# Kernel optimization log

Hardware: AMD Instinct MI355X
Metric: run time of the kernel (lower is better)

Reference implementation:

```python
import jax, jax.numpy as jnp
import numpy as np

BB, F, K, D, H, HFF, L, M_PREV = 128, 8, 256, 256, 256, 512, 2, 2


def setup_inputs() -> dict:
    key = jax.random.key(0)
    ks = jax.random.split(key, 16)
    f32 = jnp.float32

    def lin(k, fan_in, shape):
        return (jax.random.normal(k, shape, dtype=f32) / np.sqrt(fan_in)).astype(f32)

    inp = {
        "x_BD": jax.random.normal(ks[0], (BB, D), dtype=f32),
        "xhat_BFD": jax.random.normal(ks[1], (BB, F, D), dtype=f32),
        "codes_MBF": jax.random.randint(ks[2], (M_PREV, BB, 1), 0, F * K, dtype=jnp.int64),
        "codebook": jax.random.normal(ks[3], (K, D), dtype=f32) / np.sqrt(D),
        "W_in": lin(ks[4], D, (D, H)),
        "b_in": jnp.zeros((H,), f32),
        # concat projection over cat([h, xhat], -1): (H + D) -> H
        "W_cat": lin(ks[5], H + D, (H + D, H)),
        "b_cat": jnp.zeros((H,), f32),
        "W1": lin(ks[6], H, (L, H, HFF)),
        "b1": jnp.zeros((L, HFF), f32),
        "W2": lin(ks[7], HFF, (L, HFF, H)),
        "b2": jnp.zeros((L, H), f32),
        "W_out": lin(ks[8], H, (H, D)),
        "b_out": jnp.zeros((D,), f32),
    }
    return inp


def reference(x_BD, xhat_BFD, codes_MBF, codebook, W_in, b_in, W_cat, b_cat,
              W1, b1, W2, b2, W_out, b_out):
    Bb, Fb, Dd = xhat_BFD.shape
    Kk = codebook.shape[0]

    # in_proj applied to the (shared) codebook once: [K, H]
    h0 = codebook @ W_in + b_in

    # concat(h, xhat) as a linear over the concatenation, split to avoid
    # materializing a [Bb,F,K,H+D] tensor.
    Wc, Wx = W_cat[:H], W_cat[H:]
    h = (h0 @ Wc)[None, None] + (xhat_BFD @ Wx)[:, :, None] + b_cat  # [Bb,F,K,H]

    # residual MLP blocks: h <- h + W2 relu(W1 h)
    for l in range(L):
        h = h + jax.nn.relu(h @ W1[l] + b1[l]) @ W2[l] + b2[l]

    # out_proj + residual codeword (res_codeword_coeff = 1.0) + xhat offset
    cw = h @ W_out + b_out + codebook[None, None]        # [Bb,F,K,D]
    cw = cw + xhat_BFD[:, :, None]                        # reconstructed candidates

    cflat = cw.reshape(Bb, Fb * Kk, Dd)                   # [Bb, F*K, D]

    dists = (jnp.sum(x_BD * x_BD, -1, keepdims=True)
             - 2.0 * jnp.einsum('bd,bkd->bk', x_BD, cflat)
             + jnp.sum(cflat * cflat, -1))                # [Bb, F*K]

    idx = jnp.argmin(dists, axis=-1)                      # [Bb]
    xhat_next_BFD = jnp.take_along_axis(cflat, idx[:, None, None], axis=1)  # [Bb,1,D]

    codes_new = jnp.concatenate(
        [codes_MBF, idx[None, :, None].astype(codes_MBF.dtype)], axis=0)
    return xhat_next_BFD, codes_new
```

## Files before the change

kernel.cpp:

```cpp
#include <hip/hip_runtime.h>
#include <hip/hip_bf16.h>

#define B_   128
#define F_   8
#define K_   256
#define D_   256
#define H_   256
#define HFF_ 512
#define RT   64

typedef _Float16 half8  __attribute__((ext_vector_type(8)));
typedef _Float16 half4v __attribute__((ext_vector_type(4)));
typedef float floatx4   __attribute__((ext_vector_type(4)));

#define MFMAH(a,b,c) __builtin_amdgcn_mfma_f32_16x16x32_f16(a,b,c,0,0,0)

#define HA_S  260
#define HMA_S 132

__global__ void k_prep(const float* __restrict__ cb, const float* __restrict__ Win,
                       const float* __restrict__ bin, const float* __restrict__ Wcat,
                       const float* __restrict__ bcat, const float* __restrict__ xhat,
                       const float* __restrict__ W1, const float* __restrict__ W2,
                       const float* __restrict__ Wout,
                       float* __restrict__ u, float* __restrict__ v,
                       _Float16* __restrict__ w1f, _Float16* __restrict__ w2f,
                       _Float16* __restrict__ wof) {
  const int blk = blockIdx.x, t = threadIdx.x;
  if (blk < K_) {
    __shared__ float row[D_];
    __shared__ float h0row[H_];
    row[t] = cb[blk * D_ + t];
    __syncthreads();
    float acc = bin[t];
    #pragma unroll 4
    for (int i = 0; i < D_; ++i) acc = fmaf(row[i], Win[i * H_ + t], acc);
    h0row[t] = acc;
    __syncthreads();
    float acc2 = 0.f;
    #pragma unroll 4
    for (int i = 0; i < H_; ++i) acc2 = fmaf(h0row[i], Wcat[i * H_ + t], acc2);
    u[blk * H_ + t] = acc2;
  } else if (blk < K_ + B_ * F_) {
    __shared__ float row2[D_];
    const int bf = blk - K_;
    row2[t] = xhat[bf * D_ + t];
    __syncthreads();
    float acc = bcat[t];
    #pragma unroll 4
    for (int i = 0; i < D_; ++i) acc = fmaf(row2[i], Wcat[(H_ + i) * H_ + t], acc);
    v[bf * H_ + t] = acc;
  } else {
    const int e = (blk - (K_ + B_ * F_)) * 256 + t;
    const float* src; _Float16* dst; int N, NT, le;
    if (e < 262144) {
      const int layer = e >> 17; le = e & 131071;
      src = W1 + layer * (H_ * HFF_); dst = w1f + layer * (H_ * HFF_);
      N = HFF_; NT = 32;
    } else if (e < 524288) {
      const int e2 = e - 262144;
      const int layer = e2 >> 17; le = e2 & 131071;
      src = W2 + layer * (HFF_ * H_); dst = w2f + layer * (HFF_ * H_);
      N = H_; NT = 16;
    } else {
      le = e - 524288; src = Wout; dst = wof; N = D_; NT = 16;
    }
    const int jj = le & 7, lane = (le >> 3) & 63, r = le >> 9;
    const int ntile = r % NT, kstep = r / NT;
    const int row = kstep * 32 + (lane >> 4) * 8 + jj;
    const int colc = ntile * 16 + (lane & 15);
    dst[le] = (_Float16)src[row * N + colc];
  }
}

__global__ __launch_bounds__(256, 3) void k_main(
    const float* __restrict__ u, const float* __restrict__ v,
    const _Float16* __restrict__ w1f, const float* __restrict__ b1,
    const _Float16* __restrict__ w2f, const float* __restrict__ b2,
    const _Float16* __restrict__ woutf, const float* __restrict__ bout,
    const float* __restrict__ cb, const float* __restrict__ xhat,
    const float* __restrict__ x, float* __restrict__ dists) {
  __shared__ _Float16 hA[64][HA_S];
  __shared__ _Float16 hmA[64][HMA_S];
  __shared__ float x_s[D_], xh_s[D_];
  __shared__ float dist_s[4][64];

  const int t = threadIdx.x;
  const int blk = blockIdx.x;
  const int bf = blk >> 2, k0 = (blk & 3) << 6;
  const int b = bf >> 3, f = bf & 7;
  const int wave = t >> 6, lane = t & 63;
  const int col = lane & 15, quad = lane >> 4;
  const int lane8 = lane * 8;

  x_s[t]  = x[b * D_ + t];
  xh_s[t] = xhat[bf * D_ + t];

  {
    const int r = t >> 2, c0 = (t & 3) * 64;
    const float* up = u + (k0 + r) * H_ + c0;
    const float* vp = v + bf * H_ + c0;
    #pragma unroll
    for (int j = 0; j < 64; j += 8) {
      float4 uA = *(const float4*)(up + j);
      float4 vA = *(const float4*)(vp + j);
      float4 uB = *(const float4*)(up + j + 4);
      float4 vB = *(const float4*)(vp + j + 4);
      half8 hv8;
      hv8[0] = (_Float16)(uA.x + vA.x); hv8[1] = (_Float16)(uA.y + vA.y);
      hv8[2] = (_Float16)(uA.z + vA.z); hv8[3] = (_Float16)(uA.w + vA.w);
      hv8[4] = (_Float16)(uB.x + vB.x); hv8[5] = (_Float16)(uB.y + vB.y);
      hv8[6] = (_Float16)(uB.z + vB.z); hv8[7] = (_Float16)(uB.w + vB.w);
      *(half8*)&hA[r][c0 + j] = hv8;
    }
  }
  __syncthreads();

  const floatx4 zero4 = {0.f, 0.f, 0.f, 0.f};

  #pragma unroll 1
  for (int l = 0; l < 2; ++l) {
    const _Float16* w1_l = w1f + l * (H_ * HFF_);
    const _Float16* w2_l = w2f + l * (HFF_ * H_);
    const float* b1l = b1 + l * HFF_;
    const float* b2l = b2 + l * H_;

    floatx4 acc2[4][4];
    #pragma unroll
    for (int mt = 0; mt < 4; ++mt)
      #pragma unroll
      for (int nt = 0; nt < 4; ++nt) acc2[mt][nt] = zero4;

    #pragma unroll 1
    for (int ch = 0; ch < 4; ++ch) {
      floatx4 acc1[2][4];
      #pragma unroll
      for (int mt = 0; mt < 2; ++mt)
        #pragma unroll
        for (int nt = 0; nt < 4; ++nt) acc1[mt][nt] = zero4;

      const _Float16* w1_b = w1_l + (ch * 8 + wave * 2) * 512 + lane8;

      #pragma unroll 4
      for (int ks = 0; ks < 8; ++ks) {
        half8 b0 = *(const half8*)&hA[col][ks * 32 + quad * 8];
        half8 b1v = *(const half8*)&hA[16 + col][ks * 32 + quad * 8];
        half8 b2v = *(const half8*)&hA[32 + col][ks * 32 + quad * 8];
        half8 b3v = *(const half8*)&hA[48 + col][ks * 32 + quad * 8];
        const int ko = ks * 32 * 512;
        #pragma unroll
        for (int mt = 0; mt < 2; ++mt) {
          half8 aw = *(const half8*)(w1_b + ko + mt * 512);
          acc1[mt][0] = MFMAH(aw, b0, acc1[mt][0]);
          acc1[mt][1] = MFMAH(aw, b1v, acc1[mt][1]);
          acc1[mt][2] = MFMAH(aw, b2v, acc1[mt][2]);
          acc1[mt][3] = MFMAH(aw, b3v, acc1[mt][3]);
        }
      }
      #pragma unroll
      for (int mt = 0; mt < 2; ++mt) {
        const int floc = (wave * 2 + mt) * 16 + quad * 4;
        float4 bb = *(const float4*)&b1l[ch * 128 + floc];
        #pragma unroll
        for (int nt = 0; nt < 4; ++nt) {
          const int row = nt * 16 + col;
          half4v nh;
          #pragma unroll
          for (int p = 0; p < 4; ++p)
            nh[p] = (_Float16)fmaxf(acc1[mt][nt][p] + ((const float*)&bb)[p], 0.f);
          *(half4v*)&hmA[row][floc] = nh;
        }
      }
      __syncthreads();

      const _Float16* w2_b = w2_l + (ch * 64 + wave * 4) * 512 + lane8;
      #pragma unroll 2
      for (int ks = 0; ks < 4; ++ks) {
        half8 b0 = *(const half8*)&hmA[col][ks * 32 + quad * 8];
        half8 b1v = *(const half8*)&hmA[16 + col][ks * 32 + quad * 8];
        half8 b2v = *(const half8*)&hmA[32 + col][ks * 32 + quad * 8];
        half8 b3v = *(const half8*)&hmA[48 + col][ks * 32 + quad * 8];
        const int ko = ks * 16 * 512;
        #pragma unroll
        for (int mt = 0; mt < 4; ++mt) {
          half8 aw = *(const half8*)(w2_b + ko + mt * 512);
          acc2[mt][0] = MFMAH(aw, b0, acc2[mt][0]);
          acc2[mt][1] = MFMAH(aw, b1v, acc2[mt][1]);
          acc2[mt][2] = MFMAH(aw, b2v, acc2[mt][2]);
          acc2[mt][3] = MFMAH(aw, b3v, acc2[mt][3]);
        }
      }
      __syncthreads();
    }

    #pragma unroll
    for (int mt = 0; mt < 4; ++mt) {
      const int feat0 = (wave * 4 + mt) * 16 + quad * 4;
      float4 bb = *(const float4*)&b2l[feat0];
      #pragma unroll
      for (int nt = 0; nt < 4; ++nt) {
        const int row = nt * 16 + col;
        half4v oh = *(half4v*)&hA[row][feat0];
        half4v nh;
        #pragma unroll
        for (int p = 0; p < 4; ++p)
          nh[p] = (_Float16)((float)oh[p] + acc2[mt][nt][p] + ((const float*)&bb)[p]);
        *(half4v*)&hA[row][feat0] = nh;
      }
    }
    __syncthreads();
  }

  floatx4 acc3[4][4];
  #pragma unroll
  for (int mt = 0; mt < 4; ++mt)
    #pragma unroll
    for (int nt = 0; nt < 4; ++nt) acc3[mt][nt] = zero4;

  const _Float16* wo_b = woutf + (wave * 4) * 512 + lane8;
  #pragma unroll 2
  for (int ks = 0; ks < 8; ++ks) {
    half8 b0 = *(const half8*)&hA[col][ks * 32 + quad * 8];
    half8 b1v = *(const half8*)&hA[16 + col][ks * 32 + quad * 8];
    half8 b2v = *(const half8*)&hA[32 + col][ks * 32 + quad * 8];
    half8 b3v = *(const half8*)&hA[48 + col][ks * 32 + quad * 8];
    const int ko = ks * 16 * 512;
    #pragma unroll
    for (int mt = 0; mt < 4; ++mt) {
      half8 aw = *(const half8*)(wo_b + ko + mt * 512);
      acc3[mt][0] = MFMAH(aw, b0, acc3[mt][0]);
      acc3[mt][1] = MFMAH(aw, b1v, acc3[mt][1]);
      acc3[mt][2] = MFMAH(aw, b2v, acc3[mt][2]);
      acc3[mt][3] = MFMAH(aw, b3v, acc3[mt][3]);
    }
  }

  float s[4] = {0.f, 0.f, 0.f, 0.f};
  #pragma unroll
  for (int mt = 0; mt < 4; ++mt) {
    const int d0 = (wave * 4 + mt) * 16 + quad * 4;
    float4 bo = *(const float4*)&bout[d0];
    float4 xv = *(const float4*)&x_s[d0];
    float4 xh4 = *(const float4*)&xh_s[d0];
    #pragma unroll
    for (int nt = 0; nt < 4; ++nt) {
      float4 cbv = *(const float4*)&cb[(k0 + nt * 16 + col) * D_ + d0];
      #pragma unroll
      for (int p = 0; p < 4; ++p) {
        float base = ((const float*)&bo)[p] + ((const float*)&xh4)[p];
        float xx = ((const float*)&xv)[p];
        float cw = acc3[mt][nt][p] + base + ((const float*)&cbv)[p];
        s[nt] += cw * (cw - 2.f * xx);
      }
    }
  }
  #pragma unroll
  for (int nt = 0; nt < 4; ++nt) {
    s[nt] += __shfl_xor(s[nt], 16, 64);
    s[nt] += __shfl_xor(s[nt], 32, 64);
  }
  if (quad == 0) {
    #pragma unroll
    for (int nt = 0; nt < 4; ++nt)
      dist_s[wave][nt * 16 + col] = s[nt];
  }
  __syncthreads();
  if (t < 64) {
    float d = dist_s[0][t] + dist_s[1][t] + dist_s[2][t] + dist_s[3][t];
    dists[b * (F_ * K_) + f * K_ + k0 + t] = d;
  }
}

__global__ void k_top8(const float* __restrict__ dists, int* __restrict__ topi) {
  __shared__ float ds[F_ * K_];
  __shared__ float bv[256];
  __shared__ int bi_s[256];
  const int b = blockIdx.x, t = threadIdx.x;
  for (int j = t; j < F_ * K_; j += 256) ds[j] = dists[b * (F_ * K_) + j];
  __syncthreads();
  for (int pass = 0; pass < 8; ++pass) {
    float best = 3.4e38f; int bi = 0;
    for (int j = t; j < F_ * K_; j += 256) {
      const float dv = ds[j];
      if (dv < best) { best = dv; bi = j; }
    }
    bv[t] = best; bi_s[t] = bi;
    __syncthreads();
    for (int s = 128; s > 0; s >>= 1) {
      if (t < s) {
        const float ov = bv[t + s]; const int oi = bi_s[t + s];
        if (ov < bv[t] || (ov == bv[t] && oi < bi_s[t])) { bv[t] = ov; bi_s[t] = oi; }
      }
      __syncthreads();
    }
    if (t == 0) { topi[b * 8 + pass] = bi_s[0]; ds[bi_s[0]] = 3.4e38f; }
    __syncthreads();
  }
}

__global__ void k_rescore(const float* __restrict__ u, const float* __restrict__ v,
                          const float* __restrict__ W1, const float* __restrict__ b1,
                          const float* __restrict__ W2, const float* __restrict__ b2,
                          const float* __restrict__ Wout, const float* __restrict__ bout,
                          const float* __restrict__ cb, const float* __restrict__ xhat,
                          const float* __restrict__ x, const int* __restrict__ topi,
                          float* __restrict__ resc) {
  __shared__ float hs[H_];
  __shared__ float hms[HFF_];
  __shared__ float red[256];
  const int bc = blockIdx.x, t = threadIdx.x;
  const int b = bc >> 3;
  const int idx = topi[bc];
  const int f = idx >> 8, k = idx & 255;
  const int bf = b * F_ + f;

  hs[t] = u[k * H_ + t] + v[bf * H_ + t];
  __syncthreads();
  for (int l = 0; l < 2; ++l) {
    const float* W1l = W1 + l * (H_ * HFF_);
    const float* W2l = W2 + l * (HFF_ * H_);
    float a0 = b1[l * HFF_ + t], a1 = b1[l * HFF_ + 256 + t];
    for (int i = 0; i < H_; ++i) {
      const float hv = hs[i];
      a0 = fmaf(hv, W1l[i * HFF_ + t], a0);
      a1 = fmaf(hv, W1l[i * HFF_ + 256 + t], a1);
    }
    hms[t] = fmaxf(a0, 0.f);
    hms[t + 256] = fmaxf(a1, 0.f);
    __syncthreads();
    float hn = hs[t] + b2[l * H_ + t];
    for (int jj = 0; jj < HFF_; ++jj)
      hn = fmaf(hms[jj], W2l[jj * H_ + t], hn);
    __syncthreads();
    hs[t] = hn;
    __syncthreads();
  }
  float cw = bout[t] + cb[k * D_ + t] + xhat[bf * D_ + t];
  for (int i = 0; i < H_; ++i) cw = fmaf(hs[i], Wout[i * D_ + t], cw);
  red[t] = cw * (cw - 2.f * x[b * D_ + t]);
  __syncthreads();
  for (int s = 128; s > 0; s >>= 1) {
    if (t < s) red[t] += red[t + s];
    __syncthreads();
  }
  if (t == 0) resc[bc] = red[0];
}

__global__ void k_final(const float* __restrict__ u, const float* __restrict__ v,
                        const float* __restrict__ W1, const float* __restrict__ b1,
                        const float* __restrict__ W2, const float* __restrict__ b2,
                        const float* __restrict__ Wout, const float* __restrict__ bout,
                        const float* __restrict__ cb, const float* __restrict__ xhat,
                        const int* __restrict__ codes, const int* __restrict__ topi,
                        const float* __restrict__ resc, float* __restrict__ out) {
  __shared__ float hs[H_];
  __shared__ float hms[HFF_];
  __shared__ int idx_sh;
  const int b = blockIdx.x, t = threadIdx.x;
  if (t == 0) {
    float bd = 3.4e38f; int bidx = 1 << 30;
    for (int c = 0; c < 8; ++c) {
      const float d = resc[b * 8 + c];
      const int ix = topi[b * 8 + c];
      if (d < bd || (d == bd && ix < bidx)) { bd = d; bidx = ix; }
    }
    idx_sh = bidx;
  }
  __syncthreads();
  const int idx = idx_sh;
  const int f = idx >> 8, k = idx & 255;
  const int bf = b * F_ + f;

  hs[t] = u[k * H_ + t] + v[bf * H_ + t];
  __syncthreads();
  for (int l = 0; l < 2; ++l) {
    const float* W1l = W1 + l * (H_ * HFF_);
    const float* W2l = W2 + l * (HFF_ * H_);
    float a0 = b1[l * HFF_ + t], a1 = b1[l * HFF_ + 256 + t];
    for (int i = 0; i < H_; ++i) {
      const float hv = hs[i];
      a0 = fmaf(hv, W1l[i * HFF_ + t], a0);
      a1 = fmaf(hv, W1l[i * HFF_ + 256 + t], a1);
    }
    hms[t] = fmaxf(a0, 0.f);
    hms[t + 256] = fmaxf(a1, 0.f);
    __syncthreads();
    float hn = hs[t] + b2[l * H_ + t];
    for (int jj = 0; jj < HFF_; ++jj)
      hn = fmaf(hms[jj], W2l[jj * H_ + t], hn);
    __syncthreads();
    hs[t] = hn;
    __syncthreads();
  }
  float cw = bout[t] + cb[k * D_ + t] + xhat[bf * D_ + t];
  for (int i = 0; i < H_; ++i) cw = fmaf(hs[i], Wout[i * D_ + t], cw);

  out[b * D_ + t] = cw;
  if (t < 2)
    out[B_ * D_ + t * B_ + b] = (float)codes[t * B_ + b];
  else if (t == 2)
    out[B_ * D_ + 2 * B_ + b] = (float)idx;
}

extern "C" void kernel_launch(void* const* d_in, const int* in_sizes, int n_in,
                              void* d_out, int out_size, void* d_ws, size_t ws_size,
                              hipStream_t stream) {
  const float* x    = (const float*)d_in[0];
  const float* xhat = (const float*)d_in[1];
  const int*   codes= (const int*)d_in[2];
  const float* cb   = (const float*)d_in[3];
  const float* Win  = (const float*)d_in[4];
  const float* bin  = (const float*)d_in[5];
  const float* Wcat = (const float*)d_in[6];
  const float* bcat = (const float*)d_in[7];
  const float* W1   = (const float*)d_in[8];
  const float* b1   = (const float*)d_in[9];
  const float* W2   = (const float*)d_in[10];
  const float* b2   = (const float*)d_in[11];
  const float* Wout = (const float*)d_in[12];
  const float* bout = (const float*)d_in[13];
  float* out = (float*)d_out;

  float* u     = (float*)d_ws;
  float* v     = u + K_ * H_;
  float* dists = v + B_ * F_ * H_;
  float* resc  = dists + B_ * F_ * K_;
  int*   topi  = (int*)(resc + 1024);
  int*   pad   = topi + 1024;
  _Float16* w1f  = (_Float16*)(pad + 128);
  _Float16* w2f  = w1f + 2 * H_ * HFF_;
  _Float16* wof  = w2f + 2 * HFF_ * H_;

  k_prep<<<K_ + B_ * F_ + 2304, 256, 0, stream>>>(cb, Win, bin, Wcat, bcat, xhat,
                                                  W1, W2, Wout, u, v, w1f, w2f, wof);

  k_main<<<B_ * F_ * (K_ / RT), 256, 0, stream>>>(u, v, w1f, b1, w2f, b2,
                                                  wof, bout, cb, xhat, x, dists);
  k_top8<<<B_, 256, 0, stream>>>(dists, topi);
  k_rescore<<<B_ * 8, 256, 0, stream>>>(u, v, W1, b1, W2, b2, Wout, bout, cb, xhat,
                                        x, topi, resc);
  k_final<<<B_, 256, 0, stream>>>(u, v, W1, b1, W2, b2, Wout, bout, cb, xhat,
                                  codes, topi, resc, out);
}
```

Measured before the change: 562.3 us.

## Double-buffer FFN hidden chunks and widen main kernel to eight waves

```diff
diff --git a/kernel.cpp b/kernel.cpp
--- a/kernel.cpp
+++ b/kernel.cpp
@@ -73,7 +73,7 @@
   }
 }
 
-__global__ __launch_bounds__(256, 3) void k_main(
+__global__ __launch_bounds__(512, 4) void k_main(
     const float* __restrict__ u, const float* __restrict__ v,
     const _Float16* __restrict__ w1f, const float* __restrict__ b1,
     const _Float16* __restrict__ w2f, const float* __restrict__ b2,
@@ -81,9 +81,9 @@
     const float* __restrict__ cb, const float* __restrict__ xhat,
     const float* __restrict__ x, float* __restrict__ dists) {
   __shared__ _Float16 hA[64][HA_S];
-  __shared__ _Float16 hmA[64][HMA_S];
+  __shared__ _Float16 hmA[2][64][HMA_S];
   __shared__ float x_s[D_], xh_s[D_];
-  __shared__ float dist_s[4][64];
+  __shared__ float dist_s[8][64];
 
   const int t = threadIdx.x;
   const int blk = blockIdx.x;
@@ -93,15 +93,17 @@
   const int col = lane & 15, quad = lane >> 4;
   const int lane8 = lane * 8;
 
-  x_s[t]  = x[b * D_ + t];
-  xh_s[t] = xhat[bf * D_ + t];
+  if (t < D_) {
+    x_s[t]  = x[b * D_ + t];
+    xh_s[t] = xhat[bf * D_ + t];
+  }
 
   {
-    const int r = t >> 2, c0 = (t & 3) * 64;
+    const int r = t >> 3, c0 = (t & 7) * 32;
     const float* up = u + (k0 + r) * H_ + c0;
     const float* vp = v + bf * H_ + c0;
     #pragma unroll
-    for (int j = 0; j < 64; j += 8) {
+    for (int j = 0; j < 32; j += 8) {
       float4 uA = *(const float4*)(up + j);
       float4 vA = *(const float4*)(vp + j);
       float4 uB = *(const float4*)(up + j + 4);
@@ -118,6 +120,59 @@
 
   const floatx4 zero4 = {0.f, 0.f, 0.f, 0.f};
 
+  floatx4 acc2[2][4];
+
+  auto gemm1 = [&](const _Float16* __restrict__ w1_l,
+                   const float* __restrict__ b1l, const int ch,
+                   _Float16 (* __restrict__ hm)[HMA_S]) {
+    floatx4 acc1[4] = {zero4, zero4, zero4, zero4};
+    const _Float16* w1_b = w1_l + (ch * 8 + wave) * 512 + lane8;
+    #pragma unroll 4
+    for (int ks = 0; ks < 8; ++ks) {
+      half8 b0  = *(const half8*)&hA[col][ks * 32 + quad * 8];
+      half8 b1v = *(const half8*)&hA[16 + col][ks * 32 + quad * 8];
+      half8 b2v = *(const half8*)&hA[32 + col][ks * 32 + quad * 8];
+      half8 b3v = *(const half8*)&hA[48 + col][ks * 32 + quad * 8];
+      half8 aw  = *(const half8*)(w1_b + ks * 32 * 512);
+      acc1[0] = MFMAH(aw, b0,  acc1[0]);
+      acc1[1] = MFMAH(aw, b1v, acc1[1]);
+      acc1[2] = MFMAH(aw, b2v, acc1[2]);
+      acc1[3] = MFMAH(aw, b3v, acc1[3]);
+    }
+    const int floc = wave * 16 + quad * 4;
+    float4 bb = *(const float4*)&b1l[ch * 128 + floc];
+    #pragma unroll
+    for (int nt = 0; nt < 4; ++nt) {
+      const int row = nt * 16 + col;
+      half4v nh;
+      #pragma unroll
+      for (int p = 0; p < 4; ++p)
+        nh[p] = (_Float16)fmaxf(acc1[nt][p] + ((const float*)&bb)[p], 0.f);
+      *(half4v*)&hm[row][floc] = nh;
+    }
+  };
+
+  auto gemm2 = [&](const _Float16* __restrict__ w2_l, const int ch,
+                   const _Float16 (* __restrict__ hm)[HMA_S]) {
+    const _Float16* w2_b = w2_l + (ch * 64 + wave * 2) * 512 + lane8;
+    #pragma unroll 2
+    for (int ks = 0; ks < 4; ++ks) {
+      half8 b0  = *(const half8*)&hm[col][ks * 32 + quad * 8];
+      half8 b1v = *(const half8*)&hm[16 + col][ks * 32 + quad * 8];
+      half8 b2v = *(const half8*)&hm[32 + col][ks * 32 + quad * 8];
+      half8 b3v = *(const half8*)&hm[48 + col][ks * 32 + quad * 8];
+      const int ko = ks * 16 * 512;
+      #pragma unroll
+      for (int mt = 0; mt < 2; ++mt) {
+        half8 aw = *(const half8*)(w2_b + ko + mt * 512);
+        acc2[mt][0] = MFMAH(aw, b0,  acc2[mt][0]);
+        acc2[mt][1] = MFMAH(aw, b1v, acc2[mt][1]);
+        acc2[mt][2] = MFMAH(aw, b2v, acc2[mt][2]);
+        acc2[mt][3] = MFMAH(aw, b3v, acc2[mt][3]);
+      }
+    }
+  };
+
   #pragma unroll 1
   for (int l = 0; l < 2; ++l) {
     const _Float16* w1_l = w1f + l * (H_ * HFF_);
@@ -125,77 +180,25 @@
     const float* b1l = b1 + l * HFF_;
     const float* b2l = b2 + l * H_;
 
-    floatx4 acc2[4][4];
-    #pragma unroll
-    for (int mt = 0; mt < 4; ++mt)
+    #pragma unroll
+    for (int mt = 0; mt < 2; ++mt)
       #pragma unroll
       for (int nt = 0; nt < 4; ++nt) acc2[mt][nt] = zero4;
 
+    gemm1(w1_l, b1l, 0, hmA[0]);
+    __syncthreads();
+
     #pragma unroll 1
-    for (int ch = 0; ch < 4; ++ch) {
-      floatx4 acc1[2][4];
-      #pragma unroll
-      for (int mt = 0; mt < 2; ++mt)
-        #pragma unroll
-        for (int nt = 0; nt < 4; ++nt) acc1[mt][nt] = zero4;
-
-      const _Float16* w1_b = w1_l + (ch * 8 + wave * 2) * 512 + lane8;
-
-      #pragma unroll 4
-      for (int ks = 0; ks < 8; ++ks) {
-        half8 b0 = *(const half8*)&hA[col][ks * 32 + quad * 8];
-        half8 b1v = *(const half8*)&hA[16 + col][ks * 32 + quad * 8];
-        half8 b2v = *(const half8*)&hA[32 + col][ks * 32 + quad * 8];
-        half8 b3v = *(const half8*)&hA[48 + col][ks * 32 + quad * 8];
-        const int ko = ks * 32 * 512;
-        #pragma unroll
-        for (int mt = 0; mt < 2; ++mt) {
-          half8 aw = *(const half8*)(w1_b + ko + mt * 512);
-          acc1[mt][0] = MFMAH(aw, b0, acc1[mt][0]);
-          acc1[mt][1] = MFMAH(aw, b1v, acc1[mt][1]);
-          acc1[mt][2] = MFMAH(aw, b2v, acc1[mt][2]);
-          acc1[mt][3] = MFMAH(aw, b3v, acc1[mt][3]);
-        }
-      }
-      #pragma unroll
-      for (int mt = 0; mt < 2; ++mt) {
-        const int floc = (wave * 2 + mt) * 16 + quad * 4;
-        float4 bb = *(const float4*)&b1l[ch * 128 + floc];
-        #pragma unroll
-        for (int nt = 0; nt < 4; ++nt) {
-          const int row = nt * 16 + col;
-          half4v nh;
-          #pragma unroll
-          for (int p = 0; p < 4; ++p)
-            nh[p] = (_Float16)fmaxf(acc1[mt][nt][p] + ((const float*)&bb)[p], 0.f);
-          *(half4v*)&hmA[row][floc] = nh;
-        }
-      }
+    for (int ch = 0; ch < 3; ++ch) {
+      gemm1(w1_l, b1l, ch + 1, hmA[(ch + 1) & 1]);
+      gemm2(w2_l, ch, hmA[ch & 1]);
       __syncthreads();
-
-      const _Float16* w2_b = w2_l + (ch * 64 + wave * 4) * 512 + lane8;
-      #pragma unroll 2
-      for (int ks = 0; ks < 4; ++ks) {
-        half8 b0 = *(const half8*)&hmA[col][ks * 32 + quad * 8];
-        half8 b1v = *(const half8*)&hmA[16 + col][ks * 32 + quad * 8];
-        half8 b2v = *(const half8*)&hmA[32 + col][ks * 32 + quad * 8];
-        half8 b3v = *(const half8*)&hmA[48 + col][ks * 32 + quad * 8];
-        const int ko = ks * 16 * 512;
-        #pragma unroll
-        for (int mt = 0; mt < 4; ++mt) {
-          half8 aw = *(const half8*)(w2_b + ko + mt * 512);
-          acc2[mt][0] = MFMAH(aw, b0, acc2[mt][0]);
-          acc2[mt][1] = MFMAH(aw, b1v, acc2[mt][1]);
-          acc2[mt][2] = MFMAH(aw, b2v, acc2[mt][2]);
-          acc2[mt][3] = MFMAH(aw, b3v, acc2[mt][3]);
-        }
-      }
-      __syncthreads();
-    }
-
-    #pragma unroll
-    for (int mt = 0; mt < 4; ++mt) {
-      const int feat0 = (wave * 4 + mt) * 16 + quad * 4;
+    }
+    gemm2(w2_l, 3, hmA[1]);
+
+    #pragma unroll
+    for (int mt = 0; mt < 2; ++mt) {
+      const int feat0 = (wave * 2 + mt) * 16 + quad * 4;
       float4 bb = *(const float4*)&b2l[feat0];
       #pragma unroll
       for (int nt = 0; nt < 4; ++nt) {
@@ -211,24 +214,24 @@
     __syncthreads();
   }
 
-  floatx4 acc3[4][4];
+  floatx4 acc3[2][4];
   #pragma unroll
-  for (int mt = 0; mt < 4; ++mt)
+  for (int mt = 0; mt < 2; ++mt)
     #pragma unroll
     for (int nt = 0; nt < 4; ++nt) acc3[mt][nt] = zero4;
 
-  const _Float16* wo_b = woutf + (wave * 4) * 512 + lane8;
+  const _Float16* wo_b = woutf + (wave * 2) * 512 + lane8;
   #pragma unroll 2
   for (int ks = 0; ks < 8; ++ks) {
-    half8 b0 = *(const half8*)&hA[col][ks * 32 + quad * 8];
+    half8 b0  = *(const half8*)&hA[col][ks * 32 + quad * 8];
     half8 b1v = *(const half8*)&hA[16 + col][ks * 32 + quad * 8];
     half8 b2v = *(const half8*)&hA[32 + col][ks * 32 + quad * 8];
     half8 b3v = *(const half8*)&hA[48 + col][ks * 32 + quad * 8];
     const int ko = ks * 16 * 512;
     #pragma unroll
-    for (int mt = 0; mt < 4; ++mt) {
+    for (int mt = 0; mt < 2; ++mt) {
       half8 aw = *(const half8*)(wo_b + ko + mt * 512);
-      acc3[mt][0] = MFMAH(aw, b0, acc3[mt][0]);
+      acc3[mt][0] = MFMAH(aw, b0,  acc3[mt][0]);
       acc3[mt][1] = MFMAH(aw, b1v, acc3[mt][1]);
       acc3[mt][2] = MFMAH(aw, b2v, acc3[mt][2]);
       acc3[mt][3] = MFMAH(aw, b3v, acc3[mt][3]);
@@ -237,10 +240,10 @@
 
   float s[4] = {0.f, 0.f, 0.f, 0.f};
   #pragma unroll
-  for (int mt = 0; mt < 4; ++mt) {
-    const int d0 = (wave * 4 + mt) * 16 + quad * 4;
-    float4 bo = *(const float4*)&bout[d0];
-    float4 xv = *(const float4*)&x_s[d0];
+  for (int mt = 0; mt < 2; ++mt) {
+    const int d0 = (wave * 2 + mt) * 16 + quad * 4;
+    float4 bo  = *(const float4*)&bout[d0];
+    float4 xv  = *(const float4*)&x_s[d0];
     float4 xh4 = *(const float4*)&xh_s[d0];
     #pragma unroll
     for (int nt = 0; nt < 4; ++nt) {
@@ -266,7 +269,9 @@
   }
   __syncthreads();
   if (t < 64) {
-    float d = dist_s[0][t] + dist_s[1][t] + dist_s[2][t] + dist_s[3][t];
+    float d = 0.f;
+    #pragma unroll
+    for (int w = 0; w < 8; ++w) d += dist_s[w][t];
     dists[b * (F_ * K_) + f * K_ + k0 + t] = d;
   }
 }
@@ -434,7 +439,7 @@
   k_prep<<<K_ + B_ * F_ + 2304, 256, 0, stream>>>(cb, Win, bin, Wcat, bcat, xhat,
                                                   W1, W2, Wout, u, v, w1f, w2f, wof);
 
-  k_main<<<B_ * F_ * (K_ / RT), 256, 0, stream>>>(u, v, w1f, b1, w2f, b2,
+  k_main<<<B_ * F_ * (K_ / RT), 512, 0, stream>>>(u, v, w1f, b1, w2f, b2,
                                                   wof, bout, cb, xhat, x, dists);
   k_top8<<<B_, 256, 0, stream>>>(dists, topi);
   k_rescore<<<B_ * 8, 256, 0, stream>>>(u, v, W1, b1, W2, b2, Wout, bout, cb, xhat,
```

After: 918.8 us. 63.4% more time.

## Fuse rescore and final kernels into one block per batch scoring eight candidates

Applied to the files above, without the earlier changes.

```diff
diff --git a/kernel.cpp b/kernel.cpp
--- a/kernel.cpp
+++ b/kernel.cpp
@@ -298,108 +298,155 @@
   }
 }
 
-__global__ void k_rescore(const float* __restrict__ u, const float* __restrict__ v,
-                          const float* __restrict__ W1, const float* __restrict__ b1,
-                          const float* __restrict__ W2, const float* __restrict__ b2,
-                          const float* __restrict__ Wout, const float* __restrict__ bout,
-                          const float* __restrict__ cb, const float* __restrict__ xhat,
-                          const float* __restrict__ x, const int* __restrict__ topi,
-                          float* __restrict__ resc) {
-  __shared__ float hs[H_];
-  __shared__ float hms[HFF_];
-  __shared__ float red[256];
-  const int bc = blockIdx.x, t = threadIdx.x;
-  const int b = bc >> 3;
-  const int idx = topi[bc];
-  const int f = idx >> 8, k = idx & 255;
-  const int bf = b * F_ + f;
-
-  hs[t] = u[k * H_ + t] + v[bf * H_ + t];
-  __syncthreads();
+#define NC 8
+__global__ __launch_bounds__(256) void k_resfin(
+    const float* __restrict__ u, const float* __restrict__ v,
+    const float* __restrict__ W1, const float* __restrict__ b1,
+    const float* __restrict__ W2, const float* __restrict__ b2,
+    const float* __restrict__ Wout, const float* __restrict__ bout,
+    const float* __restrict__ cb, const float* __restrict__ xhat,
+    const float* __restrict__ x, const int* __restrict__ codes,
+    const int* __restrict__ topi, float* __restrict__ out) {
+  __shared__ float hs8[NC][H_ + 4];
+  __shared__ float hms8[NC][HFF_ + 4];
+  __shared__ float cw8[NC][H_ + 4];
+  __shared__ float redw[4][NC];
+  __shared__ int   idx_sh;
+
+  const int b = blockIdx.x, t = threadIdx.x;
+  const int wave = t >> 6, lane = t & 63;
+
+  int kc[NC], bfc[NC], ixc[NC];
+  #pragma unroll
+  for (int c = 0; c < NC; ++c) {
+    const int ix = topi[b * 8 + c];
+    ixc[c] = ix;
+    kc[c] = ix & 255;
+    bfc[c] = b * F_ + (ix >> 8);
+  }
+
+  #pragma unroll
+  for (int c = 0; c < NC; ++c)
+    hs8[c][t] = u[kc[c] * H_ + t] + v[bfc[c] * H_ + t];
+  __syncthreads();
+
+  #pragma unroll 1
   for (int l = 0; l < 2; ++l) {
     const float* W1l = W1 + l * (H_ * HFF_);
     const float* W2l = W2 + l * (HFF_ * H_);
-    float a0 = b1[l * HFF_ + t], a1 = b1[l * HFF_ + 256 + t];
-    for (int i = 0; i < H_; ++i) {
-      const float hv = hs[i];
-      a0 = fmaf(hv, W1l[i * HFF_ + t], a0);
-      a1 = fmaf(hv, W1l[i * HFF_ + 256 + t], a1);
-    }
-    hms[t] = fmaxf(a0, 0.f);
-    hms[t + 256] = fmaxf(a1, 0.f);
-    __syncthreads();
-    float hn = hs[t] + b2[l * H_ + t];
-    for (int jj = 0; jj < HFF_; ++jj)
-      hn = fmaf(hms[jj], W2l[jj * H_ + t], hn);
-    __syncthreads();
-    hs[t] = hn;
-    __syncthreads();
-  }
-  float cw = bout[t] + cb[k * D_ + t] + xhat[bf * D_ + t];
-  for (int i = 0; i < H_; ++i) cw = fmaf(hs[i], Wout[i * D_ + t], cw);
-  red[t] = cw * (cw - 2.f * x[b * D_ + t]);
-  __syncthreads();
-  for (int s = 128; s > 0; s >>= 1) {
-    if (t < s) red[t] += red[t + s];
-    __syncthreads();
-  }
-  if (t == 0) resc[bc] = red[0];
-}
-
-__global__ void k_final(const float* __restrict__ u, const float* __restrict__ v,
-                        const float* __restrict__ W1, const float* __restrict__ b1,
-                        const float* __restrict__ W2, const float* __restrict__ b2,
-                        const float* __restrict__ Wout, const float* __restrict__ bout,
-                        const float* __restrict__ cb, const float* __restrict__ xhat,
-                        const int* __restrict__ codes, const int* __restrict__ topi,
-                        const float* __restrict__ resc, float* __restrict__ out) {
-  __shared__ float hs[H_];
-  __shared__ float hms[HFF_];
-  __shared__ int idx_sh;
-  const int b = blockIdx.x, t = threadIdx.x;
+
+    float a0[NC], a1[NC];
+    {
+      const float bb0 = b1[l * HFF_ + t], bb1 = b1[l * HFF_ + 256 + t];
+      #pragma unroll
+      for (int c = 0; c < NC; ++c) { a0[c] = bb0; a1[c] = bb1; }
+    }
+    #pragma unroll 2
+    for (int i = 0; i < H_; i += 4) {
+      float4 hv[NC];
+      #pragma unroll
+      for (int c = 0; c < NC; ++c) hv[c] = *(const float4*)&hs8[c][i];
+      #pragma unroll
+      for (int q = 0; q < 4; ++q) {
+        const float w0 = W1l[(i + q) * HFF_ + t];
+        const float w1 = W1l[(i + q) * HFF_ + 256 + t];
+        #pragma unroll
+        for (int c = 0; c < NC; ++c) {
+          const float h = ((const float*)&hv[c])[q];
+          a0[c] = fmaf(h, w0, a0[c]);
+          a1[c] = fmaf(h, w1, a1[c]);
+        }
+      }
+    }
+    #pragma unroll
+    for (int c = 0; c < NC; ++c) {
+      hms8[c][t] = fmaxf(a0[c], 0.f);
+      hms8[c][t + 256] = fmaxf(a1[c], 0.f);
+    }
+    __syncthreads();
+
+    float hn[NC];
+    {
+      const float bb2 = b2[l * H_ + t];
+      #pragma unroll
+      for (int c = 0; c < NC; ++c) hn[c] = hs8[c][t] + bb2;
+    }
+    #pragma unroll 2
+    for (int jj = 0; jj < HFF_; jj += 4) {
+      float4 hv[NC];
+      #pragma unroll
+      for (int c = 0; c < NC; ++c) hv[c] = *(const float4*)&hms8[c][jj];
+      #pragma unroll
+      for (int q = 0; q < 4; ++q) {
+        const float w = W2l[(jj + q) * H_ + t];
+        #pragma unroll
+        for (int c = 0; c < NC; ++c)
+          hn[c] = fmaf(((const float*)&hv[c])[q], w, hn[c]);
+      }
+    }
+    __syncthreads();
+    #pragma unroll
+    for (int c = 0; c < NC; ++c) hs8[c][t] = hn[c];
+    __syncthreads();
+  }
+
+  float cw[NC];
+  {
+    const float bo = bout[t];
+    #pragma unroll
+    for (int c = 0; c < NC; ++c)
+      cw[c] = bo + cb[kc[c] * D_ + t] + xhat[bfc[c] * D_ + t];
+  }
+  #pragma unroll 2
+  for (int i = 0; i < H_; i += 4) {
+    float4 hv[NC];
+    #pragma unroll
+    for (int c = 0; c < NC; ++c) hv[c] = *(const float4*)&hs8[c][i];
+    #pragma unroll
+    for (int q = 0; q < 4; ++q) {
+      const float w = Wout[(i + q) * D_ + t];
+      #pragma unroll
+      for (int c = 0; c < NC; ++c)
+        cw[c] = fmaf(((const float*)&hv[c])[q], w, cw[c]);
+    }
+  }
+
+  const float xx = x[b * D_ + t];
+  float p[NC];
+  #pragma unroll
+  for (int c = 0; c < NC; ++c) {
+    cw8[c][t] = cw[c];
+    p[c] = cw[c] * (cw[c] - 2.f * xx);
+  }
+  #pragma unroll
+  for (int c = 0; c < NC; ++c) {
+    float vsum = p[c];
+    vsum += __shfl_xor(vsum, 1, 64);
+    vsum += __shfl_xor(vsum, 2, 64);
+    vsum += __shfl_xor(vsum, 4, 64);
+    vsum += __shfl_xor(vsum, 8, 64);
+    vsum += __shfl_xor(vsum, 16, 64);
+    vsum += __shfl_xor(vsum, 32, 64);
+    if (lane == 0) redw[wave][c] = vsum;
+  }
+  __syncthreads();
   if (t == 0) {
-    float bd = 3.4e38f; int bidx = 1 << 30;
-    for (int c = 0; c < 8; ++c) {
-      const float d = resc[b * 8 + c];
-      const int ix = topi[b * 8 + c];
-      if (d < bd || (d == bd && ix < bidx)) { bd = d; bidx = ix; }
-    }
-    idx_sh = bidx;
-  }
-  __syncthreads();
-  const int idx = idx_sh;
-  const int f = idx >> 8, k = idx & 255;
-  const int bf = b * F_ + f;
-
-  hs[t] = u[k * H_ + t] + v[bf * H_ + t];
-  __syncthreads();
-  for (int l = 0; l < 2; ++l) {
-    const float* W1l = W1 + l * (H_ * HFF_);
-    const float* W2l = W2 + l * (HFF_ * H_);
-    float a0 = b1[l * HFF_ + t], a1 = b1[l * HFF_ + 256 + t];
-    for (int i = 0; i < H_; ++i) {
-      const float hv = hs[i];
-      a0 = fmaf(hv, W1l[i * HFF_ + t], a0);
-      a1 = fmaf(hv, W1l[i * HFF_ + 256 + t], a1);
-    }
-    hms[t] = fmaxf(a0, 0.f);
-    hms[t + 256] = fmaxf(a1, 0.f);
-    __syncthreads();
-    float hn = hs[t] + b2[l * H_ + t];
-    for (int jj = 0; jj < HFF_; ++jj)
-      hn = fmaf(hms[jj], W2l[jj * H_ + t], hn);
-    __syncthreads();
-    hs[t] = hn;
-    __syncthreads();
-  }
-  float cw = bout[t] + cb[k * D_ + t] + xhat[bf * D_ + t];
-  for (int i = 0; i < H_; ++i) cw = fmaf(hs[i], Wout[i * D_ + t], cw);
-
-  out[b * D_ + t] = cw;
+    float bd = 3.4e38f; int bidx = 1 << 30; int bc = 0;
+    #pragma unroll
+    for (int c = 0; c < NC; ++c) {
+      const float d = redw[0][c] + redw[1][c] + redw[2][c] + redw[3][c];
+      if (d < bd || (d == bd && ixc[c] < bidx)) { bd = d; bidx = ixc[c]; bc = c; }
+    }
+    idx_sh = bc;
+  }
+  __syncthreads();
+  const int cwin = idx_sh;
+
+  out[b * D_ + t] = cw8[cwin][t];
   if (t < 2)
     out[B_ * D_ + t * B_ + b] = (float)codes[t * B_ + b];
   else if (t == 2)
-    out[B_ * D_ + 2 * B_ + b] = (float)idx;
+    out[B_ * D_ + 2 * B_ + b] = (float)ixc[cwin];
 }
 
 extern "C" void kernel_launch(void* const* d_in, const int* in_sizes, int n_in,
@@ -437,8 +484,6 @@
   k_main<<<B_ * F_ * (K_ / RT), 256, 0, stream>>>(u, v, w1f, b1, w2f, b2,
                                                   wof, bout, cb, xhat, x, dists);
   k_top8<<<B_, 256, 0, stream>>>(dists, topi);
-  k_rescore<<<B_ * 8, 256, 0, stream>>>(u, v, W1, b1, W2, b2, Wout, bout, cb, xhat,
-                                        x, topi, resc);
-  k_final<<<B_, 256, 0, stream>>>(u, v, W1, b1, W2, b2, Wout, bout, cb, xhat,
-                                  codes, topi, resc, out);
+  k_resfin<<<B_, 256, 0, stream>>>(u, v, W1, b1, W2, b2, Wout, bout, cb, xhat,
+                                   x, codes, topi, out);
 }
```

Measured after the change: 634.1 us. 12.8% more time.
